# Kernel optimization log

Hardware: AMD Instinct MI355X
Metric: run time of the kernel (lower is better)

Reference implementation:

```python
import math
import jax, jax.numpy as jnp
import numpy as np

B, T, D_MODEL, H, D = 2, 1024, 1024, 16, 64
NUM_LEVELS = int(math.ceil(math.log2(T + 1))) + 1  # 12 for max_seq_len=1024


def _fenwick_level(idx):
    return (idx & -idx).bit_length() - 1


def build_fenwick_masks(T, num_levels):
    """NumPy replica of the torch build_fenwick_masks; returns [L, T, T] float32."""
    j_to_nodes = {}
    for j in range(1, T + 1):
        nodes = []
        idx = j
        while idx <= T:
            nodes.append((idx, _fenwick_level(idx)))
            idx += idx & -idx
        j_to_nodes[j] = nodes
    t_to_query_nodes = {}
    for t in range(1, T + 1):
        s = set()
        idx = t
        while idx > 0:
            s.add(idx)
            idx -= idx & -idx
        t_to_query_nodes[t] = s
    masks = np.zeros((num_levels, T, T), dtype=np.float32)
    for t in range(1, T + 1):
        qn = t_to_query_nodes[t]
        for j in range(1, t + 1):
            for node_idx, node_level in j_to_nodes[j]:
                if node_idx in qn:
                    masks[min(node_level, num_levels - 1), t - 1, j - 1] = 1.0
                    break
    return masks


def setup_inputs() -> dict:
    key = jax.random.key(0)
    ks = jax.random.split(key, 8)
    s = 0.02
    return {
        "x": jax.random.normal(ks[0], (B, T, D_MODEL), jnp.float32),
        "qw": jax.random.normal(ks[1], (D_MODEL, H * D), jnp.float32) * s,
        "qb": jnp.zeros((H * D,), jnp.float32),
        "kw": jax.random.normal(ks[2], (D_MODEL, H * D), jnp.float32) * s,
        "kb": jnp.zeros((H * D,), jnp.float32),
        "vw": jax.random.normal(ks[3], (D_MODEL, H * D), jnp.float32) * s,
        "vb": jnp.zeros((H * D,), jnp.float32),
        "lw": jax.random.normal(ks[4], (D_MODEL, H * NUM_LEVELS), jnp.float32) * s,
        "lb": jnp.zeros((H * NUM_LEVELS,), jnp.float32),
        "ow": jax.random.normal(ks[5], (H * D, D_MODEL), jnp.float32) * s,
        "ob": jnp.zeros((D_MODEL,), jnp.float32),
        "level_masks": jnp.asarray(build_fenwick_masks(T, NUM_LEVELS)),
    }


def reference(x, qw, qb, kw, kb, vw, vb, lw, lb, ow, ob, level_masks):
    b, t, _ = x.shape
    phi = lambda a: jax.nn.elu(a) + 1.0  # ELU+1 feature map
    # projections -> [B, H, T, D]
    Q = (x @ qw + qb).reshape(b, t, H, D).transpose(0, 2, 1, 3)
    K = (x @ kw + kb).reshape(b, t, H, D).transpose(0, 2, 1, 3)
    V = (x @ vw + vb).reshape(b, t, H, D).transpose(0, 2, 1, 3)
    Qp, Kp = phi(Q), phi(K)
    # per-level mixing weights: [B, H, T, L]
    logits = (x @ lw + lb).reshape(b, t, H, NUM_LEVELS).transpose(0, 2, 1, 3)
    w = jax.nn.softmax(logits, axis=-1)
    # scores are level-independent in the original; compute once
    S = jnp.einsum('bhid,bhjd->bhij', Qp, Kp)
    # sum_l w_l * mask_l folded into one weighted mask: [B, H, T, T]
    Mw = jnp.einsum('bhil,lij->bhij', w, level_masks)
    Sm = S * Mw
    num = jnp.einsum('bhij,bhjd->bhid', Sm, V)
    den = jnp.maximum(jnp.sum(Sm, axis=-1, keepdims=True), 1e-6)
    out = (num / den).transpose(0, 2, 1, 3).reshape(b, t, H * D)
    return out @ ow + ob
```

## Files before the change

kernel.cpp:

```cpp
#include <hip/hip_runtime.h>
#include <math.h>

typedef __bf16 bf16;
typedef __attribute__((ext_vector_type(4))) __bf16 bf16x4;
typedef __attribute__((ext_vector_type(8))) __bf16 bf16x8;
typedef __attribute__((ext_vector_type(4))) float f32x4;

#define B_SZ 2
#define T_SZ 1024
#define DM_SZ 1024
#define H_SZ 16
#define D_SZ 64
#define L_SZ 12
#define M_ROWS 2048
#define N_PAD 3328

__device__ __forceinline__ f32x4 mfma_16x16x32(bf16x8 a, bf16x8 b, f32x4 c) {
  return __builtin_amdgcn_mfma_f32_16x16x32_bf16(a, b, c, 0, 0, 0);
}

__device__ __forceinline__ void gload_lds16(const bf16* g, bf16* l) {
  __builtin_amdgcn_global_load_lds((const __attribute__((address_space(1))) void*)g,
                                   (__attribute__((address_space(3))) void*)l,
                                   16, 0, 0);
}

__global__ __launch_bounds__(256) void k_prep(
    const float* __restrict__ x, bf16* __restrict__ xb,
    const float* __restrict__ qw, const float* __restrict__ kw,
    const float* __restrict__ vw, const float* __restrict__ ow,
    const float* __restrict__ lw,
    bf16* __restrict__ wqkvT, bf16* __restrict__ owT) {
  const int z = blockIdx.z;
  const int t = threadIdx.x;
  if (z == 5) {
    const size_t base = ((size_t)blockIdx.y * 16 + blockIdx.x) * 8192 + t * 32;
#pragma unroll
    for (int u = 0; u < 4; ++u) {
      const float* p = x + base + u * 8;
      f32x4 a = *(const f32x4*)p;
      f32x4 b = *(const f32x4*)(p + 4);
      bf16x8 o;
#pragma unroll
      for (int e = 0; e < 4; ++e) { o[e] = (bf16)a[e]; o[e + 4] = (bf16)b[e]; }
      *(bf16x8*)(xb + base + u * 8) = o;
    }
    return;
  }
  __shared__ __align__(16) bf16 tile[64][66];
  const float* in; bf16* out; int C = 1024;
  if (z == 0)      { in = qw; out = wqkvT; }
  else if (z == 1) { in = kw; out = wqkvT + (size_t)1024 * DM_SZ; }
  else if (z == 2) { in = vw; out = wqkvT + (size_t)2048 * DM_SZ; }
  else if (z == 3) { in = ow; out = owT; }
  else             { in = lw; out = wqkvT + (size_t)3072 * DM_SZ; C = 192;
                     if (blockIdx.x >= 3) return; }
  const int tc = blockIdx.x * 64;
  const int tr = blockIdx.y * 64;
  const int r = t >> 2;
  const int c4 = (t & 3) << 4;
  const float* src = in + (size_t)(tr + r) * C + tc + c4;
  f32x4 f0 = *(const f32x4*)(src);
  f32x4 f1 = *(const f32x4*)(src + 4);
  f32x4 f2 = *(const f32x4*)(src + 8);
  f32x4 f3 = *(const f32x4*)(src + 12);
#pragma unroll
  for (int e = 0; e < 4; ++e) {
    tile[r][c4 + e]      = (bf16)f0[e];
    tile[r][c4 + 4 + e]  = (bf16)f1[e];
    tile[r][c4 + 8 + e]  = (bf16)f2[e];
    tile[r][c4 + 12 + e] = (bf16)f3[e];
  }
  __syncthreads();
  bf16x8 w0, w1;
#pragma unroll
  for (int e = 0; e < 8; ++e) { w0[e] = tile[c4 + e][r]; w1[e] = tile[c4 + 8 + e][r]; }
  bf16* dst = out + (size_t)(tc + r) * DM_SZ + tr + c4;
  *(bf16x8*)(dst) = w0;
  *(bf16x8*)(dst + 8) = w1;
}

__global__ __launch_bounds__(256) void k_gemm_qkvl(
    const bf16* __restrict__ A, const bf16* __restrict__ Wt,
    const float* __restrict__ qb, const float* __restrict__ kb,
    const float* __restrict__ vb, const float* __restrict__ lb,
    bf16* __restrict__ Qp, bf16* __restrict__ Kp,
    bf16* __restrict__ VTg, float* __restrict__ logit) {
  __shared__ __align__(16) char smem[34816];
  bf16* As = (bf16*)smem;
  bf16* Bs = As + 8192;
  const int nb = blockIdx.x * 128;
  const int mb = blockIdx.y * 128;
  const int t = threadIdx.x;
  const int wv = t >> 6;
  const int lane = t & 63;
  const int l16 = lane & 15;
  const int quad = lane >> 4;
  const int wm = (wv & 1) * 64;
  const int wn = (wv >> 1) * 64;

  const int trow = t >> 3;
  const int tcol = (t & 7) * 8;

  const f32x4 zero4 = {0.f, 0.f, 0.f, 0.f};
  f32x4 acc[4][4];
#pragma unroll
  for (int i = 0; i < 4; ++i)
#pragma unroll
    for (int j = 0; j < 4; ++j) acc[i][j] = zero4;

  const bf16* ag = A + (size_t)(mb + trow) * DM_SZ + tcol;
  const bf16* bg = Wt + (size_t)(nb + trow) * DM_SZ + tcol;

  for (int k0 = 0; k0 < DM_SZ; k0 += 64) {
    __syncthreads();
#pragma unroll
    for (int i = 0; i < 4; ++i)
      gload_lds16(ag + (size_t)i * 32 * DM_SZ + k0, As + i * 2048 + t * 8);
#pragma unroll
    for (int i = 0; i < 4; ++i)
      gload_lds16(bg + (size_t)i * 32 * DM_SZ + k0, Bs + i * 2048 + t * 8);
    __syncthreads();
#pragma unroll
    for (int ks = 0; ks < 2; ++ks) {
      bf16x8 af[4];
#pragma unroll
      for (int mi = 0; mi < 4; ++mi)
        af[mi] = *(const bf16x8*)(As + (wm + mi * 16 + l16) * 64 + ks * 32 + quad * 8);
#pragma unroll
      for (int ni = 0; ni < 4; ++ni) {
        bf16x8 bfr = *(const bf16x8*)(Bs + (wn + ni * 16 + l16) * 64 + ks * 32 + quad * 8);
#pragma unroll
        for (int mi = 0; mi < 4; ++mi)
          acc[mi][ni] = mfma_16x16x32(af[mi], bfr, acc[mi][ni]);
      }
    }
  }

  const int seg = nb >> 10;
  if (seg < 2) {
    const float* bias = seg == 0 ? qb : kb;
    bf16* outp = seg == 0 ? Qp : Kp;
    const int c0 = (nb & 1023) + wn;
#pragma unroll
    for (int ni = 0; ni < 4; ++ni) {
      const int col = c0 + ni * 16 + l16;
      const float bv = bias[col];
#pragma unroll
      for (int mi = 0; mi < 4; ++mi) {
#pragma unroll
        for (int r = 0; r < 4; ++r) {
          const int row = mb + wm + mi * 16 + quad * 4 + r;
          float v = acc[mi][ni][r] + bv;
          v = (v > 0.f) ? (v + 1.f) : __expf(v);
          outp[(size_t)row * DM_SZ + col] = (bf16)v;
        }
      }
    }
  } else if (seg == 2) {
    bf16* Trt = (bf16*)smem;
    const int cb = nb - 2048;
    __syncthreads();
#pragma unroll
    for (int ni = 0; ni < 4; ++ni) {
      const int nloc = wn + ni * 16 + l16;
      const float bv = vb[cb + nloc];
#pragma unroll
      for (int mi = 0; mi < 4; ++mi) {
        const int mloc = wm + mi * 16 + quad * 4;
        bf16x4 pk;
#pragma unroll
        for (int r = 0; r < 4; ++r) pk[r] = (bf16)(acc[mi][ni][r] + bv);
        *(bf16x4*)&Trt[nloc * 136 + mloc] = pk;
      }
    }
    __syncthreads();
    const int dn = t >> 1, ch = t & 1;
    const int bq = mb >> 10;
    const int m0g = mb & 1023;
    bf16* dst = VTg + ((size_t)(bq * 1024 + cb + dn)) * T_SZ + m0g + ch * 64;
    const bf16* srcl = Trt + dn * 136 + ch * 64;
#pragma unroll
    for (int e = 0; e < 8; ++e)
      *(bf16x8*)(dst + e * 8) = *(const bf16x8*)(srcl + e * 8);
  } else {
    const int lc0 = (nb - 3072) + wn;
#pragma unroll
    for (int ni = 0; ni < 4; ++ni) {
      const int lcol = lc0 + ni * 16 + l16;
      if (lcol < H_SZ * L_SZ) {
        const float bv = lb[lcol];
#pragma unroll
        for (int mi = 0; mi < 4; ++mi) {
#pragma unroll
          for (int r = 0; r < 4; ++r) {
            const int row = mb + wm + mi * 16 + quad * 4 + r;
            logit[(size_t)row * (H_SZ * L_SZ) + lcol] = acc[mi][ni][r] + bv;
          }
        }
      }
    }
  }
}

__global__ __launch_bounds__(256) void k_attn(const bf16* __restrict__ Qp,
                                              const bf16* __restrict__ Kp,
                                              const bf16* __restrict__ VTg,
                                              const float* __restrict__ Lg,
                                              bf16* __restrict__ O) {
  __shared__ __align__(16) bf16 Ks[2][64 * 64];
  __shared__ __align__(16) bf16 VTs[2][64 * 64];
  __shared__ __align__(16) bf16 Pl[4][16][80];
  __shared__ float Ws[64 * L_SZ];

  const int idx = blockIdx.x;
  const int s = idx >> 5;
  const int bh = idx & 31;
  const int it = (s < 8) ? (15 - s) : (s - 8);
  const int b = bh >> 4;
  const int h = bh & 15;
  const int i0 = it * 64;
  const int t = threadIdx.x;
  const int wv = t >> 6;
  const int lane = t & 63;
  const int l16 = lane & 15;
  const int quad = lane >> 4;
  const int m0 = wv * 16;

  const size_t base_bt = (size_t)b * T_SZ;

  const int st_r0  = wv * 16 + (lane >> 3);
  const int st_cs  = (((lane & 7) ^ (lane >> 3)) << 3);
  const int st_lds = wv * 1024 + lane * 8;
  const bf16* kbase = Kp + (base_bt + st_r0) * DM_SZ + h * 64 + st_cs;
  const bf16* vbase = VTg + ((size_t)bh * 64 + st_r0) * T_SZ + st_cs;

  auto stage = [&](int jt, int buf) {
    const int j0s = jt * 64;
    const bf16* kg = kbase + (size_t)j0s * DM_SZ;
    gload_lds16(kg, &Ks[buf][st_lds]);
    gload_lds16(kg + (size_t)8 * DM_SZ, &Ks[buf][st_lds + 512]);
    const bf16* vg = vbase + j0s;
    gload_lds16(vg, &VTs[buf][st_lds]);
    gload_lds16(vg + (size_t)8 * T_SZ, &VTs[buf][st_lds + 512]);
  };

  stage(0, 0);

  const bf16* qptr = Qp + (base_bt + i0 + m0 + l16) * DM_SZ + h * 64 + quad * 8;
  const bf16x8 aq0 = *(const bf16x8*)(qptr);
  const bf16x8 aq1 = *(const bf16x8*)(qptr + 32);

  if (t < 64) {
    const float* lp = Lg + (base_bt + i0 + t) * (H_SZ * L_SZ) + h * L_SZ;
    float v[L_SZ];
    float m = -1e30f;
#pragma unroll
    for (int l = 0; l < L_SZ; ++l) { v[l] = lp[l]; m = fmaxf(m, v[l]); }
    float sum = 0.f;
#pragma unroll
    for (int l = 0; l < L_SZ; ++l) { v[l] = __expf(v[l] - m); sum += v[l]; }
    const float inv = 1.f / sum;
#pragma unroll
    for (int l = 0; l < L_SZ; ++l) Ws[t * L_SZ + l] = v[l] * inv;
  }

  const f32x4 zero4 = {0.f, 0.f, 0.f, 0.f};
  f32x4 accn[4];
#pragma unroll
  for (int tn = 0; tn < 4; ++tn) accn[tn] = zero4;
  float den[4] = {0.f, 0.f, 0.f, 0.f};

  const int il_base = m0 + quad * 4;
  const int rsw = (l16 & 7) << 3;

  for (int jt = 0; jt <= it; ++jt) {
    const int cur = jt & 1;
    __syncthreads();
    if (jt < it) stage(jt + 1, cur ^ 1);

    f32x4 sacc[4];
    __builtin_amdgcn_s_setprio(1);
#pragma unroll
    for (int tn = 0; tn < 4; ++tn) {
      sacc[tn] = zero4;
      const int rb = (tn * 16 + l16) * 64;
      bf16x8 bk0 = *(const bf16x8*)&Ks[cur][rb + ((quad * 8) ^ rsw)];
      bf16x8 bk1 = *(const bf16x8*)&Ks[cur][rb + ((32 + quad * 8) ^ rsw)];
      sacc[tn] = mfma_16x16x32(aq0, bk0, sacc[tn]);
      sacc[tn] = mfma_16x16x32(aq1, bk1, sacc[tn]);
    }
    __builtin_amdgcn_s_setprio(0);

    const int j0 = jt * 64;
    if (jt < it) {
      const int lvlA = 6 + (31 - __clz((unsigned)(it ^ jt)));
      const int lvlB = 6 + (31 - __clz((unsigned)((it + 1) ^ jt)));
      float wrow[4];
#pragma unroll
      for (int r = 0; r < 4; ++r) {
        const int il = il_base + r;
        wrow[r] = Ws[il * L_SZ + ((il == 63) ? lvlB : lvlA)];
      }
#pragma unroll
      for (int tn = 0; tn < 4; ++tn) {
#pragma unroll
        for (int r = 0; r < 4; ++r) {
          const float p = sacc[tn][r] * wrow[r];
          den[r] += p;
          Pl[wv][quad * 4 + r][(tn * 16 + l16) ^ (quad << 4)] = (bf16)p;
        }
      }
    } else {
#pragma unroll
      for (int tn = 0; tn < 4; ++tn) {
#pragma unroll
        for (int r = 0; r < 4; ++r) {
          const int il = il_base + r;
          const int ig = i0 + il;
          const int jg = j0 + tn * 16 + l16;
          float p = 0.f;
          if (jg <= ig) {
            const int lvl = 31 - __clz((unsigned)((ig + 1) ^ jg));
            p = sacc[tn][r] * Ws[il * L_SZ + lvl];
          }
          den[r] += p;
          Pl[wv][quad * 4 + r][(tn * 16 + l16) ^ (quad << 4)] = (bf16)p;
        }
      }
    }

    __builtin_amdgcn_s_setprio(1);
#pragma unroll
    for (int ks = 0; ks < 2; ++ks) {
      bf16x8 apf = *(const bf16x8*)&Pl[wv][l16][(ks * 32 + quad * 8) ^ ((l16 >> 2) << 4)];
#pragma unroll
      for (int tn = 0; tn < 4; ++tn) {
        bf16x8 bvf = *(const bf16x8*)&VTs[cur][(tn * 16 + l16) * 64 +
                                              ((ks * 32 + quad * 8) ^ rsw)];
        accn[tn] = mfma_16x16x32(apf, bvf, accn[tn]);
      }
    }
    __builtin_amdgcn_s_setprio(0);
  }

#pragma unroll
  for (int r = 0; r < 4; ++r) {
    float d = den[r];
    d += __shfl_xor(d, 1, 64);
    d += __shfl_xor(d, 2, 64);
    d += __shfl_xor(d, 4, 64);
    d += __shfl_xor(d, 8, 64);
    den[r] = fmaxf(d, 1e-6f);
  }

#pragma unroll
  for (int tn = 0; tn < 4; ++tn) {
#pragma unroll
    for (int r = 0; r < 4; ++r) {
      const int il = il_base + r;
      O[(base_bt + i0 + il) * DM_SZ + h * 64 + tn * 16 + l16] =
          (bf16)(accn[tn][r] / den[r]);
    }
  }
}

__global__ __launch_bounds__(256) void k_gemm_out(const bf16* __restrict__ A,
                                                  const bf16* __restrict__ Wt,
                                                  const float* __restrict__ ob,
                                                  float* __restrict__ out) {
  __shared__ __align__(16) bf16 As[2][64 * 64];
  __shared__ __align__(16) bf16 Bs[2][64 * 64];
  const int nb = blockIdx.x * 64;
  const int mb = blockIdx.y * 64;
  const int t = threadIdx.x;
  const int wv = t >> 6;
  const int lane = t & 63;
  const int l16 = lane & 15;
  const int quad = lane >> 4;
  const int wm = wv * 16;

  const int trow = t >> 3;
  const int tcol = (t & 7) * 8;

  const f32x4 zero4 = {0.f, 0.f, 0.f, 0.f};
  f32x4 acc[4];
#pragma unroll
  for (int j = 0; j < 4; ++j) acc[j] = zero4;

  const bf16* ag = A + (size_t)(mb + trow) * DM_SZ + tcol;
  const bf16* bg = Wt + (size_t)(nb + trow) * DM_SZ + tcol;

  auto stageg = [&](int k0, int buf) {
    gload_lds16(ag + k0, As[buf] + t * 8);
    gload_lds16(ag + (size_t)32 * DM_SZ + k0, As[buf] + 2048 + t * 8);
    gload_lds16(bg + k0, Bs[buf] + t * 8);
    gload_lds16(bg + (size_t)32 * DM_SZ + k0, Bs[buf] + 2048 + t * 8);
  };

  stageg(0, 0);
  for (int k0 = 0; k0 < DM_SZ; k0 += 64) {
    const int cur = (k0 >> 6) & 1;
    __syncthreads();
    if (k0 + 64 < DM_SZ) stageg(k0 + 64, cur ^ 1);
#pragma unroll
    for (int ks = 0; ks < 2; ++ks) {
      bf16x8 af = *(const bf16x8*)(As[cur] + (wm + l16) * 64 + ks * 32 + quad * 8);
#pragma unroll
      for (int ni = 0; ni < 4; ++ni) {
        bf16x8 bfr = *(const bf16x8*)(Bs[cur] + (ni * 16 + l16) * 64 + ks * 32 + quad * 8);
        acc[ni] = mfma_16x16x32(af, bfr, acc[ni]);
      }
    }
  }
#pragma unroll
  for (int ni = 0; ni < 4; ++ni) {
    const int col = nb + ni * 16 + l16;
    const float bv = ob[col];
#pragma unroll
    for (int r = 0; r < 4; ++r) {
      const int row = mb + wm + quad * 4 + r;
      out[(size_t)row * DM_SZ + col] = acc[ni][r] + bv;
    }
  }
}

extern "C" void kernel_launch(void* const* d_in, const int* in_sizes, int n_in,
                              void* d_out, int out_size, void* d_ws, size_t ws_size,
                              hipStream_t stream) {
  (void)in_sizes; (void)n_in; (void)out_size; (void)ws_size;
  const float* x  = (const float*)d_in[0];
  const float* qw = (const float*)d_in[1];
  const float* qb = (const float*)d_in[2];
  const float* kw = (const float*)d_in[3];
  const float* kb = (const float*)d_in[4];
  const float* vw = (const float*)d_in[5];
  const float* vb = (const float*)d_in[6];
  const float* lw = (const float*)d_in[7];
  const float* lb = (const float*)d_in[8];
  const float* ow = (const float*)d_in[9];
  const float* ob = (const float*)d_in[10];

  char* ws = (char*)d_ws;
  size_t off = 0;
  auto alloc = [&](size_t bytes) -> char* {
    char* p = ws + off;
    off += (bytes + 255) & ~(size_t)255;
    return p;
  };
  bf16* xb     = (bf16*)alloc((size_t)M_ROWS * DM_SZ * 2);
  bf16* wqkvT  = (bf16*)alloc((size_t)N_PAD * DM_SZ * 2);
  bf16* owT    = (bf16*)alloc((size_t)DM_SZ * DM_SZ * 2);
  bf16* Qp     = (bf16*)alloc((size_t)M_ROWS * DM_SZ * 2);
  bf16* Kpb    = (bf16*)alloc((size_t)M_ROWS * DM_SZ * 2);
  bf16* VTg    = (bf16*)alloc((size_t)M_ROWS * DM_SZ * 2);
  bf16* attn   = (bf16*)alloc((size_t)M_ROWS * DM_SZ * 2);
  float* logit = (float*)alloc((size_t)M_ROWS * H_SZ * L_SZ * 4);

  const dim3 blk(256);
  k_prep<<<dim3(16, 16, 6), blk, 0, stream>>>(x, xb, qw, kw, vw, ow, lw, wqkvT, owT);
  k_gemm_qkvl<<<dim3(N_PAD / 128, M_ROWS / 128), blk, 0, stream>>>(
      xb, wqkvT, qb, kb, vb, lb, Qp, Kpb, VTg, logit);
  k_attn<<<dim3((T_SZ / 64) * B_SZ * H_SZ), blk, 0, stream>>>(Qp, Kpb, VTg, logit, attn);
  k_gemm_out<<<dim3(DM_SZ / 64, M_ROWS / 64), blk, 0, stream>>>(attn, owT, ob, (float*)d_out);
}
```

Baseline: 184.5 us.

## Replace quadratic off-diagonal attention with per-tile KV state sums and double-buffer QKV GEMM

Adds a k_build kernel that computes a per-64-token-tile outer-product state K^T V and a key sum. The attention kernel then handles every off-diagonal tile through level-grouped prefix sums of these states, as linear attention, and only computes the diagonal tile explicitly. Row 63 of each tile has a different level assignment, so it gets special handling. The QKV GEMM also moves to double-buffered LDS staging. This removes the O(T^2) score work, at the cost of an extra launch, reading fp32 state buffers of up to 16 tiles per block, and rounding the summed states to bf16.

```diff
diff --git a/kernel.cpp b/kernel.cpp
--- a/kernel.cpp
+++ b/kernel.cpp
@@ -86,9 +86,9 @@
     const float* __restrict__ vb, const float* __restrict__ lb,
     bf16* __restrict__ Qp, bf16* __restrict__ Kp,
     bf16* __restrict__ VTg, float* __restrict__ logit) {
-  __shared__ __align__(16) char smem[34816];
-  bf16* As = (bf16*)smem;
-  bf16* Bs = As + 8192;
+  __shared__ __align__(16) char smem[65536];
+  bf16* Asb = (bf16*)smem;
+  bf16* Bsb = Asb + 16384;
   const int nb = blockIdx.x * 128;
   const int mb = blockIdx.y * 128;
   const int t = threadIdx.x;
@@ -112,15 +112,24 @@
   const bf16* ag = A + (size_t)(mb + trow) * DM_SZ + tcol;
   const bf16* bg = Wt + (size_t)(nb + trow) * DM_SZ + tcol;
 
-  for (int k0 = 0; k0 < DM_SZ; k0 += 64) {
-    __syncthreads();
+  auto stage = [&](int k0, int buf) {
+    bf16* As = Asb + buf * 8192;
+    bf16* Bs = Bsb + buf * 8192;
 #pragma unroll
     for (int i = 0; i < 4; ++i)
       gload_lds16(ag + (size_t)i * 32 * DM_SZ + k0, As + i * 2048 + t * 8);
 #pragma unroll
     for (int i = 0; i < 4; ++i)
       gload_lds16(bg + (size_t)i * 32 * DM_SZ + k0, Bs + i * 2048 + t * 8);
+  };
+
+  stage(0, 0);
+  for (int k0 = 0; k0 < DM_SZ; k0 += 64) {
+    const int cur = (k0 >> 6) & 1;
     __syncthreads();
+    if (k0 + 64 < DM_SZ) stage(k0 + 64, cur ^ 1);
+    const bf16* As = Asb + cur * 8192;
+    const bf16* Bs = Bsb + cur * 8192;
 #pragma unroll
     for (int ks = 0; ks < 2; ++ks) {
       bf16x8 af[4];
@@ -203,15 +212,76 @@
   }
 }
 
+__global__ __launch_bounds__(256) void k_build(const bf16* __restrict__ Kp,
+                                               const bf16* __restrict__ VTg,
+                                               float* __restrict__ Hbuf,
+                                               float* __restrict__ ksumbuf) {
+  __shared__ __align__(16) bf16 KTs[64][72];
+  __shared__ __align__(16) bf16 VTs[64][72];
+  const int idx = blockIdx.x;
+  const int bh = idx & 31;
+  const int jt = idx >> 5;
+  const int b = bh >> 4, h = bh & 15;
+  const int t = threadIdx.x;
+  const int wv = t >> 6, lane = t & 63, l16 = lane & 15, quad = lane >> 4;
+  const int r = t >> 2, c = (t & 3) << 4;
+
+  const bf16* vp = VTg + ((size_t)bh * 64 + r) * T_SZ + jt * 64 + c;
+  bf16x8 v0 = *(const bf16x8*)vp;
+  bf16x8 v1 = *(const bf16x8*)(vp + 8);
+  const bf16* kp = Kp + ((size_t)b * T_SZ + jt * 64 + r) * DM_SZ + h * 64 + c;
+  bf16x8 k0 = *(const bf16x8*)kp;
+  bf16x8 k1 = *(const bf16x8*)(kp + 8);
+  *(bf16x8*)&VTs[r][c] = v0;
+  *(bf16x8*)&VTs[r][c + 8] = v1;
+#pragma unroll
+  for (int e = 0; e < 8; ++e) { KTs[c + e][r] = k0[e]; KTs[c + 8 + e][r] = k1[e]; }
+  __syncthreads();
+
+  if (t < 64) {
+    float s = 0.f;
+#pragma unroll
+    for (int j = 0; j < 64; ++j) s += (float)KTs[t][j];
+    ksumbuf[((size_t)bh * 16 + jt) * 64 + t] = s;
+  }
+
+  const f32x4 zero4 = {0.f, 0.f, 0.f, 0.f};
+  f32x4 acc[4];
+#pragma unroll
+  for (int tn = 0; tn < 4; ++tn) acc[tn] = zero4;
+#pragma unroll
+  for (int ks = 0; ks < 2; ++ks) {
+    bf16x8 af = *(const bf16x8*)&VTs[wv * 16 + l16][ks * 32 + quad * 8];
+#pragma unroll
+    for (int tn = 0; tn < 4; ++tn) {
+      bf16x8 bfr = *(const bf16x8*)&KTs[tn * 16 + l16][ks * 32 + quad * 8];
+      acc[tn] = mfma_16x16x32(af, bfr, acc[tn]);
+    }
+  }
+  float* hp = Hbuf + ((size_t)bh * 16 + jt) * 4096;
+#pragma unroll
+  for (int tn = 0; tn < 4; ++tn)
+#pragma unroll
+    for (int rr = 0; rr < 4; ++rr)
+      hp[(wv * 16 + quad * 4 + rr) * 64 + tn * 16 + l16] = acc[tn][rr];
+}
+
 __global__ __launch_bounds__(256) void k_attn(const bf16* __restrict__ Qp,
                                               const bf16* __restrict__ Kp,
                                               const bf16* __restrict__ VTg,
                                               const float* __restrict__ Lg,
+                                              const float* __restrict__ Hbuf,
+                                              const float* __restrict__ ksumbuf,
                                               bf16* __restrict__ O) {
-  __shared__ __align__(16) bf16 Ks[2][64 * 64];
-  __shared__ __align__(16) bf16 VTs[2][64 * 64];
+  __shared__ __align__(16) bf16 Ks[64][72];
+  __shared__ __align__(16) bf16 VTs[64][72];
+  __shared__ __align__(16) bf16 Ms[4][64][72];
   __shared__ __align__(16) bf16 Pl[4][16][80];
+  __shared__ __align__(16) bf16 Bdvs[16][72];
   __shared__ float Ws[64 * L_SZ];
+  __shared__ float q63s[64];
+  __shared__ float y63s[64];
+  __shared__ float dsum63s;
 
   const int idx = blockIdx.x;
   const int s = idx >> 5;
@@ -226,30 +296,26 @@
   const int l16 = lane & 15;
   const int quad = lane >> 4;
   const int m0 = wv * 16;
-
   const size_t base_bt = (size_t)b * T_SZ;
 
-  const int st_r0  = wv * 16 + (lane >> 3);
-  const int st_cs  = (((lane & 7) ^ (lane >> 3)) << 3);
-  const int st_lds = wv * 1024 + lane * 8;
-  const bf16* kbase = Kp + (base_bt + st_r0) * DM_SZ + h * 64 + st_cs;
-  const bf16* vbase = VTg + ((size_t)bh * 64 + st_r0) * T_SZ + st_cs;
-
-  auto stage = [&](int jt, int buf) {
-    const int j0s = jt * 64;
-    const bf16* kg = kbase + (size_t)j0s * DM_SZ;
-    gload_lds16(kg, &Ks[buf][st_lds]);
-    gload_lds16(kg + (size_t)8 * DM_SZ, &Ks[buf][st_lds + 512]);
-    const bf16* vg = vbase + j0s;
-    gload_lds16(vg, &VTs[buf][st_lds]);
-    gload_lds16(vg + (size_t)8 * T_SZ, &VTs[buf][st_lds + 512]);
-  };
-
-  stage(0, 0);
+  for (int i = t; i < 16 * 72; i += 256) ((short*)Bdvs)[i] = 0;
+  if (t < 64) y63s[t] = 0.f;
+  if (t == 0) dsum63s = 0.f;
 
   const bf16* qptr = Qp + (base_bt + i0 + m0 + l16) * DM_SZ + h * 64 + quad * 8;
   const bf16x8 aq0 = *(const bf16x8*)(qptr);
   const bf16x8 aq1 = *(const bf16x8*)(qptr + 32);
+
+  if (t < 64) q63s[t] = (float)Qp[(base_bt + i0 + 63) * DM_SZ + h * 64 + t];
+
+  const int sr = t >> 2;
+  const int sc = (t & 3) << 4;
+  const bf16* kpg = Kp + (base_bt + i0 + sr) * DM_SZ + h * 64 + sc;
+  const bf16x8 kv0 = *(const bf16x8*)(kpg);
+  const bf16x8 kv1 = *(const bf16x8*)(kpg + 8);
+  const bf16* vpg = VTg + ((size_t)bh * 64 + sr) * T_SZ + i0 + sc;
+  const bf16x8 vv0 = *(const bf16x8*)(vpg);
+  const bf16x8 vv1 = *(const bf16x8*)(vpg + 8);
 
   if (t < 64) {
     const float* lp = Lg + (base_bt + i0 + t) * (H_SZ * L_SZ) + h * L_SZ;
@@ -265,79 +331,164 @@
     for (int l = 0; l < L_SZ; ++l) Ws[t * L_SZ + l] = v[l] * inv;
   }
 
+  __syncthreads();
+
+  *(bf16x8*)&Ks[sr][sc] = kv0;
+  *(bf16x8*)&Ks[sr][sc + 8] = kv1;
+  *(bf16x8*)&VTs[sr][sc] = vv0;
+  *(bf16x8*)&VTs[sr][sc + 8] = vv1;
+
+  const int il_base = m0 + quad * 4;
   const f32x4 zero4 = {0.f, 0.f, 0.f, 0.f};
   f32x4 accn[4];
 #pragma unroll
   for (int tn = 0; tn < 4; ++tn) accn[tn] = zero4;
   float den[4] = {0.f, 0.f, 0.f, 0.f};
 
-  const int il_base = m0 + quad * 4;
-  const int rsw = (l16 & 7) << 3;
-
-  for (int jt = 0; jt <= it; ++jt) {
-    const int cur = jt & 1;
-    __syncthreads();
-    if (jt < it) stage(jt + 1, cur ^ 1);
-
+  if (it > 0) {
+    const float* hb = Hbuf + (size_t)bh * 16 * 4096;
+    const float* ksb = ksumbuf + (size_t)bh * 16 * 64;
+    f32x4 m63a[4];
+#pragma unroll
+    for (int i = 0; i < 4; ++i) m63a[i] = zero4;
+    float dv63 = 0.f;
+    int x = it;
+    while (x > 0) {
+      const int g = __builtin_ctz((unsigned)x);
+      const int lo = x - (1 << g);
+      f32x4 ma[4];
+#pragma unroll
+      for (int i = 0; i < 4; ++i) ma[i] = zero4;
+      float dva = 0.f;
+      for (int jt = lo; jt < x; ++jt) {
+        const float wB = Ws[63 * L_SZ + 6 + (31 - __clz((unsigned)((it + 1) ^ jt)))];
+        const float* lp = hb + jt * 4096 + t * 16;
+#pragma unroll
+        for (int i = 0; i < 4; ++i) {
+          f32x4 hv = *(const f32x4*)(lp + i * 4);
+#pragma unroll
+          for (int e = 0; e < 4; ++e) {
+            ma[i][e] += hv[e];
+            m63a[i][e] += wB * hv[e];
+          }
+        }
+        if (t < 64) {
+          const float ksv = ksb[jt * 64 + t];
+          dva += ksv;
+          dv63 += wB * ksv;
+        }
+      }
+      bf16x8 o0, o1;
+#pragma unroll
+      for (int e = 0; e < 4; ++e) {
+        o0[e] = (bf16)ma[0][e]; o0[e + 4] = (bf16)ma[1][e];
+        o1[e] = (bf16)ma[2][e]; o1[e + 4] = (bf16)ma[3][e];
+      }
+      *(bf16x8*)&Ms[g][t >> 2][(t & 3) << 4] = o0;
+      *(bf16x8*)&Ms[g][t >> 2][((t & 3) << 4) + 8] = o1;
+      if (t < 64) Bdvs[g][t] = (bf16)dva;
+      x = lo;
+    }
+    float p63 = 0.f;
+    const int d1b = (t & 3) << 4;
+#pragma unroll
+    for (int i = 0; i < 4; ++i)
+#pragma unroll
+      for (int e = 0; e < 4; ++e) p63 += q63s[d1b + i * 4 + e] * m63a[i][e];
+    p63 += __shfl_xor(p63, 1, 64);
+    p63 += __shfl_xor(p63, 2, 64);
+    if ((t & 3) == 0) y63s[t >> 2] = p63;
+    if (t < 64) {
+      float pd = q63s[t] * dv63;
+      pd += __shfl_xor(pd, 1, 64);
+      pd += __shfl_xor(pd, 2, 64);
+      pd += __shfl_xor(pd, 4, 64);
+      pd += __shfl_xor(pd, 8, 64);
+      pd += __shfl_xor(pd, 16, 64);
+      pd += __shfl_xor(pd, 32, 64);
+      if (t == 0) dsum63s = pd;
+    }
+  }
+  __syncthreads();
+
+  if (it > 0) {
+    int x = it;
+    while (x > 0) {
+      const int g = __builtin_ctz((unsigned)x);
+      f32x4 ya[4];
+#pragma unroll
+      for (int tn = 0; tn < 4; ++tn) ya[tn] = zero4;
+#pragma unroll
+      for (int ks = 0; ks < 2; ++ks) {
+        const bf16x8 af = ks ? aq1 : aq0;
+#pragma unroll
+        for (int tn = 0; tn < 4; ++tn) {
+          bf16x8 bfr = *(const bf16x8*)&Ms[g][tn * 16 + l16][ks * 32 + quad * 8];
+          ya[tn] = mfma_16x16x32(af, bfr, ya[tn]);
+        }
+      }
+      float wg[4];
+#pragma unroll
+      for (int r = 0; r < 4; ++r) {
+        const int il = il_base + r;
+        wg[r] = (il == 63) ? 0.f : Ws[il * L_SZ + 6 + g];
+      }
+#pragma unroll
+      for (int tn = 0; tn < 4; ++tn)
+#pragma unroll
+        for (int r = 0; r < 4; ++r) accn[tn][r] += wg[r] * ya[tn][r];
+      x -= 1 << g;
+    }
+    f32x4 da = zero4;
+#pragma unroll
+    for (int ks = 0; ks < 2; ++ks) {
+      const bf16x8 af = ks ? aq1 : aq0;
+      bf16x8 bfr = *(const bf16x8*)&Bdvs[l16][ks * 32 + quad * 8];
+      da = mfma_16x16x32(af, bfr, da);
+    }
+#pragma unroll
+    for (int r = 0; r < 4; ++r) {
+      const int il = il_base + r;
+      const float wd = (il == 63) ? 0.f : Ws[il * L_SZ + 6 + (l16 & 3)];
+      den[r] += wd * da[r];
+    }
+  }
+
+  {
     f32x4 sacc[4];
     __builtin_amdgcn_s_setprio(1);
 #pragma unroll
     for (int tn = 0; tn < 4; ++tn) {
       sacc[tn] = zero4;
-      const int rb = (tn * 16 + l16) * 64;
-      bf16x8 bk0 = *(const bf16x8*)&Ks[cur][rb + ((quad * 8) ^ rsw)];
-      bf16x8 bk1 = *(const bf16x8*)&Ks[cur][rb + ((32 + quad * 8) ^ rsw)];
+      bf16x8 bk0 = *(const bf16x8*)&Ks[tn * 16 + l16][quad * 8];
+      bf16x8 bk1 = *(const bf16x8*)&Ks[tn * 16 + l16][32 + quad * 8];
       sacc[tn] = mfma_16x16x32(aq0, bk0, sacc[tn]);
       sacc[tn] = mfma_16x16x32(aq1, bk1, sacc[tn]);
     }
     __builtin_amdgcn_s_setprio(0);
-
-    const int j0 = jt * 64;
-    if (jt < it) {
-      const int lvlA = 6 + (31 - __clz((unsigned)(it ^ jt)));
-      const int lvlB = 6 + (31 - __clz((unsigned)((it + 1) ^ jt)));
-      float wrow[4];
+#pragma unroll
+    for (int tn = 0; tn < 4; ++tn) {
 #pragma unroll
       for (int r = 0; r < 4; ++r) {
         const int il = il_base + r;
-        wrow[r] = Ws[il * L_SZ + ((il == 63) ? lvlB : lvlA)];
-      }
-#pragma unroll
-      for (int tn = 0; tn < 4; ++tn) {
-#pragma unroll
-        for (int r = 0; r < 4; ++r) {
-          const float p = sacc[tn][r] * wrow[r];
-          den[r] += p;
-          Pl[wv][quad * 4 + r][(tn * 16 + l16) ^ (quad << 4)] = (bf16)p;
+        const int ig = i0 + il;
+        const int jg = i0 + tn * 16 + l16;
+        float p = 0.f;
+        if (jg <= ig) {
+          const int lvl = 31 - __clz((unsigned)((ig + 1) ^ jg));
+          p = sacc[tn][r] * Ws[il * L_SZ + lvl];
         }
-      }
-    } else {
-#pragma unroll
-      for (int tn = 0; tn < 4; ++tn) {
-#pragma unroll
-        for (int r = 0; r < 4; ++r) {
-          const int il = il_base + r;
-          const int ig = i0 + il;
-          const int jg = j0 + tn * 16 + l16;
-          float p = 0.f;
-          if (jg <= ig) {
-            const int lvl = 31 - __clz((unsigned)((ig + 1) ^ jg));
-            p = sacc[tn][r] * Ws[il * L_SZ + lvl];
-          }
-          den[r] += p;
-          Pl[wv][quad * 4 + r][(tn * 16 + l16) ^ (quad << 4)] = (bf16)p;
-        }
-      }
-    }
-
+        den[r] += p;
+        Pl[wv][quad * 4 + r][(tn * 16 + l16) ^ (quad << 4)] = (bf16)p;
+      }
+    }
     __builtin_amdgcn_s_setprio(1);
 #pragma unroll
     for (int ks = 0; ks < 2; ++ks) {
       bf16x8 apf = *(const bf16x8*)&Pl[wv][l16][(ks * 32 + quad * 8) ^ ((l16 >> 2) << 4)];
 #pragma unroll
       for (int tn = 0; tn < 4; ++tn) {
-        bf16x8 bvf = *(const bf16x8*)&VTs[cur][(tn * 16 + l16) * 64 +
-                                              ((ks * 32 + quad * 8) ^ rsw)];
+        bf16x8 bvf = *(const bf16x8*)&VTs[tn * 16 + l16][ks * 32 + quad * 8];
         accn[tn] = mfma_16x16x32(apf, bvf, accn[tn]);
       }
     }
@@ -351,16 +502,21 @@
     d += __shfl_xor(d, 2, 64);
     d += __shfl_xor(d, 4, 64);
     d += __shfl_xor(d, 8, 64);
-    den[r] = fmaxf(d, 1e-6f);
-  }
+    den[r] = d;
+  }
+  if (il_base + 3 == 63) den[3] += dsum63s;
+#pragma unroll
+  for (int r = 0; r < 4; ++r) den[r] = fmaxf(den[r], 1e-6f);
 
 #pragma unroll
   for (int tn = 0; tn < 4; ++tn) {
 #pragma unroll
     for (int r = 0; r < 4; ++r) {
       const int il = il_base + r;
+      float v = accn[tn][r];
+      if (il == 63) v += y63s[tn * 16 + l16];
       O[(base_bt + i0 + il) * DM_SZ + h * 64 + tn * 16 + l16] =
-          (bf16)(accn[tn][r] / den[r]);
+          (bf16)(v / den[r]);
     }
   }
 }
@@ -456,11 +612,15 @@
   bf16* VTg    = (bf16*)alloc((size_t)M_ROWS * DM_SZ * 2);
   bf16* attn   = (bf16*)alloc((size_t)M_ROWS * DM_SZ * 2);
   float* logit = (float*)alloc((size_t)M_ROWS * H_SZ * L_SZ * 4);
+  float* Hbuf  = (float*)alloc((size_t)32 * 16 * 4096 * 4);
+  float* ksumb = (float*)alloc((size_t)32 * 16 * 64 * 4);
 
   const dim3 blk(256);
   k_prep<<<dim3(16, 16, 6), blk, 0, stream>>>(x, xb, qw, kw, vw, ow, lw, wqkvT, owT);
   k_gemm_qkvl<<<dim3(N_PAD / 128, M_ROWS / 128), blk, 0, stream>>>(
       xb, wqkvT, qb, kb, vb, lb, Qp, Kpb, VTg, logit);
-  k_attn<<<dim3((T_SZ / 64) * B_SZ * H_SZ), blk, 0, stream>>>(Qp, Kpb, VTg, logit, attn);
+  k_build<<<dim3(32 * 16), blk, 0, stream>>>(Kpb, VTg, Hbuf, ksumb);
+  k_attn<<<dim3((T_SZ / 64) * B_SZ * H_SZ), blk, 0, stream>>>(
+      Qp, Kpb, VTg, logit, Hbuf, ksumb, attn);
   k_gemm_out<<<dim3(DM_SZ / 64, M_ROWS / 64), blk, 0, stream>>>(attn, owT, ob, (float*)d_out);
 }
```

After: 179.4 us. -2.7%, faster.
